# Optimization experiments

Hardware: AMD Instinct MI355X
Metric: run time of the kernel (lower is better)

## Reference

```python
import jax, jax.numpy as jnp
import numpy as np

B, T, C = 4, 2048, 1024
E = 8            # n_expert
K = 2            # n_expert_per_token
H = 1408         # moe_intermediate_size
HS = 1408 * 2    # shared expert intermediate (moe_intermediate_size * n_shared_expert)


def setup_inputs() -> dict:
    key = jax.random.key(0)
    k = jax.random.split(key, 8)
    s = 0.02
    return {
        "x":   jax.random.normal(k[0], (B, T, C), jnp.float32),
        "Wg":  jax.random.normal(k[1], (C, E), jnp.float32) * s,      # router gate
        "W1":  jax.random.normal(k[2], (E, C, H), jnp.float32) * s,   # fc_1 per expert
        "W2":  jax.random.normal(k[3], (E, C, H), jnp.float32) * s,   # fc_2 per expert
        "W3":  jax.random.normal(k[4], (E, H, C), jnp.float32) * s,   # proj per expert
        "Ws1": jax.random.normal(k[5], (C, HS), jnp.float32) * s,     # shared fc_1
        "Ws2": jax.random.normal(k[6], (C, HS), jnp.float32) * s,     # shared fc_2
        "Ws3": jax.random.normal(k[7], (HS, C), jnp.float32) * s,     # shared proj
    }


def reference(x, Wg, W1, W2, W3, Ws1, Ws2, Ws3):
    b, t, c = x.shape
    xf = x.reshape(-1, c)                       # [N, C]
    n = xf.shape[0]

    # Router: top-k then softmax over the selected logits (float32 softmax).
    router = xf @ Wg                            # [N, E]
    top_logits, idx = jax.lax.top_k(router, K)  # [N, K]
    probs = jax.nn.softmax(top_logits.astype(jnp.float32), axis=-1).astype(x.dtype)

    # token_expert_weights: scatter probs into dense [N, E] per-expert weights.
    w = jnp.zeros((n, E), x.dtype).at[jnp.arange(n)[:, None], idx].add(probs)

    # Per-expert gated MLP on all tokens; zero-weight tokens contribute nothing,
    # matching the masked gather/scatter-add of the original.
    h = jax.nn.silu(jnp.einsum('tc,ech->eth', xf, W1)) * jnp.einsum('tc,ech->eth', xf, W2)
    y = jnp.einsum('eth,ehc,te->tc', h, W3, w)  # weighted combine
    y = y.reshape(b, t, c)

    # Shared expert on the residual input.
    hs = jax.nn.silu(xf @ Ws1) * (xf @ Ws2)     # [N, HS]
    y = y + (hs @ Ws3).reshape(b, t, c)
    return y
```

## Files before the change

### kernel.cpp

```cpp
#include <hip/hip_runtime.h>
#include <cstdint>

#define NTOK 8192
#define CDIM 1024
#define HDIM 1408
#define HSDIM 2816
#define NEXP 8

typedef __attribute__((ext_vector_type(8))) short s8v;
typedef __attribute__((ext_vector_type(4))) float f4v;
typedef __attribute__((ext_vector_type(8))) unsigned short u16x8;

__device__ __forceinline__ unsigned short f2bf(float f) {
    unsigned int u = __float_as_uint(f);
    unsigned int r = (u + 0x7fffu + ((u >> 16) & 1u)) >> 16;
    return (unsigned short)r;
}
__device__ __forceinline__ float bf2f(unsigned short u) {
    return __uint_as_float(((unsigned int)u) << 16);
}

__device__ __forceinline__ void gld_lds16(const unsigned short* g, unsigned short* l) {
    __builtin_amdgcn_global_load_lds(
        (const __attribute__((address_space(1))) void*)g,
        (__attribute__((address_space(3))) void*)l, 16, 0, 0);
}


#define P_RTR 2048
#define P_CVT 8192
#define P_T1 (22 * 16 * 16)
#define P_T2 (16 * 22 * 8)
#define P_T3 (44 * 16 * 2)
#define P_T4 (16 * 44 * 1)
#define P_TOTAL (P_RTR + P_CVT + P_T1 + P_T2 + P_T3 + P_T4)

__device__ __forceinline__ void transpose_tile(
    float (*T)[68], const float* __restrict__ in, unsigned short* __restrict__ out,
    int R, int Cc, int bx, int by) {
    const int t = threadIdx.x;
    const int r0 = by * 64, c0 = bx * 64;
    {
        const int rl = t >> 2, cq = t & 3;
        const float* src = in + (size_t)(r0 + rl) * Cc + c0;
#pragma unroll
        for (int i = 0; i < 4; i++) {
            float4 v = *(const float4*)(src + (cq + 4 * i) * 4);
            *(float4*)&T[rl][(cq + 4 * i) * 4] = v;
        }
    }
    __syncthreads();
    {
        const int cl = t >> 2, rq = t & 3;
        unsigned short* dst = out + (size_t)(c0 + cl) * R + r0 + rq * 16;
        u16x8 lo, hi;
#pragma unroll
        for (int j = 0; j < 8; j++) lo[j] = f2bf(T[rq * 16 + j][cl]);
#pragma unroll
        for (int j = 0; j < 8; j++) hi[j] = f2bf(T[rq * 16 + 8 + j][cl]);
        *(u16x8*)dst = lo;
        *(u16x8*)(dst + 8) = hi;
    }
}

__global__ __launch_bounds__(256) void prep_kernel(
    const float* __restrict__ x, const float* __restrict__ Wg,
    const float* __restrict__ W1, const float* __restrict__ W2, const float* __restrict__ W3,
    const float* __restrict__ Ws1, const float* __restrict__ Ws2, const float* __restrict__ Ws3,
    unsigned short* __restrict__ xb,
    unsigned short* __restrict__ w1t, unsigned short* __restrict__ w2t,
    unsigned short* __restrict__ w3t,
    unsigned short* __restrict__ ws1t, unsigned short* __restrict__ ws2t,
    unsigned short* __restrict__ ws3t,
    int* __restrict__ idxK, float* __restrict__ probK, int* __restrict__ meta) {
    __shared__ float T[64][68];
    int bid = blockIdx.x;
    const int tid = threadIdx.x;

    if (bid < P_RTR) {
        const int t = bid * 4 + (tid >> 6);
        const int lane = tid & 63;
        const float* xr = x + (size_t)t * CDIM;
        float acc[NEXP];
#pragma unroll
        for (int e = 0; e < NEXP; e++) acc[e] = 0.f;
        for (int c = lane; c < CDIM; c += 64) {
            float xv = xr[c];
            const float* wr = Wg + c * NEXP;
#pragma unroll
            for (int e = 0; e < NEXP; e++) acc[e] += xv * wr[e];
        }
#pragma unroll
        for (int e = 0; e < NEXP; e++)
            for (int off = 32; off > 0; off >>= 1)
                acc[e] += __shfl_down(acc[e], off, 64);
        if (lane == 0) {
            int b0 = 0; float v0 = acc[0];
#pragma unroll
            for (int e = 1; e < NEXP; e++) if (acc[e] > v0) { v0 = acc[e]; b0 = e; }
            int b1 = -1; float v1 = -1e30f;
#pragma unroll
            for (int e = 0; e < NEXP; e++) if (e != b0 && acc[e] > v1) { v1 = acc[e]; b1 = e; }
            float p0 = 1.f / (1.f + __expf(v1 - v0));
            idxK[2 * t] = b0; idxK[2 * t + 1] = b1;
            probK[2 * t] = p0; probK[2 * t + 1] = 1.f - p0;
            atomicAdd(&meta[b0], 1);
            atomicAdd(&meta[b1], 1);
        }
        return;
    }
    bid -= P_RTR;
    if (bid < P_CVT) {
        const int i = bid * 256 + tid;
        float4 v = ((const float4*)x)[i];
        ushort4 o;
        o.x = f2bf(v.x); o.y = f2bf(v.y); o.z = f2bf(v.z); o.w = f2bf(v.w);
        ((ushort4*)xb)[i] = o;
        return;
    }
    bid -= P_CVT;
    if (bid < P_T1) {
        const int bx = bid % 22, by = (bid / 22) % 16, z = bid / (22 * 16);
        const float* in = (z < 8) ? W1 : W2;
        unsigned short* out = (z < 8) ? w1t : w2t;
        const int zz = (z < 8) ? z : z - 8;
        const size_t bs = (size_t)CDIM * HDIM;
        transpose_tile(T, in + zz * bs, out + zz * bs, CDIM, HDIM, bx, by);
        return;
    }
    bid -= P_T1;
    if (bid < P_T2) {
        const int bx = bid % 16, by = (bid / 16) % 22, z = bid / (16 * 22);
        const size_t bs = (size_t)HDIM * CDIM;
        transpose_tile(T, W3 + z * bs, w3t + z * bs, HDIM, CDIM, bx, by);
        return;
    }
    bid -= P_T2;
    if (bid < P_T3) {
        const int bx = bid % 44, by = (bid / 44) % 16, z = bid / (44 * 16);
        const float* in = (z == 0) ? Ws1 : Ws2;
        unsigned short* out = (z == 0) ? ws1t : ws2t;
        transpose_tile(T, in, out, CDIM, HSDIM, bx, by);
        return;
    }
    bid -= P_T3;
    {
        const int bx = bid % 16, by = bid / 16;
        transpose_tile(T, Ws3, ws3t, HSDIM, CDIM, bx, by);
    }
}

__global__ void offsets_kernel(int* meta) {
    int s = 0;
    for (int e = 0; e < NEXP; e++) { meta[8 + e] = s; meta[16 + e] = s; s += meta[e]; }
}

__global__ void fill_kernel(const int* __restrict__ idxK, const float* __restrict__ probK,
                            int* __restrict__ meta, int* __restrict__ rowT, float* __restrict__ rowW,
                            int* __restrict__ tokSlot) {
    int t = blockIdx.x * 256 + threadIdx.x;
    if (t >= NTOK) return;
#pragma unroll
    for (int k = 0; k < 2; k++) {
        int e = idxK[2 * t + k];
        int p = atomicAdd(&meta[16 + e], 1);
        rowT[p] = t;
        rowW[p] = probK[2 * t + k];
        tokSlot[2 * t + k] = p;
    }
}

__global__ __launch_bounds__(256) void gemm12_kernel(
    const unsigned short* __restrict__ xb,
    const unsigned short* __restrict__ w1, const unsigned short* __restrict__ w2,
    const unsigned short* __restrict__ ws1, const unsigned short* __restrict__ ws2,
    unsigned short* __restrict__ hE, unsigned short* __restrict__ hS,
    const int* __restrict__ rowT, const int* __restrict__ meta) {
    const int id = blockIdx.x;
    int z, m0, n0; bool SH;
    if (id < 3520) { SH = false; z = id & 7; int q = id >> 3; m0 = (q % 20) * 128; n0 = (q / 20) * 64; }
    else           { SH = true;  z = 8; int q = id - 3520; m0 = (q & 63) * 128; n0 = (q >> 6) * 64; }
    const int M = SH ? NTOK : meta[z];
    const int base = SH ? 0 : meta[8 + z];
    if (m0 >= M) return;

    const unsigned short* B1 = SH ? ws1 : w1 + (size_t)z * HDIM * CDIM;
    const unsigned short* B2 = SH ? ws2 : w2 + (size_t)z * HDIM * CDIM;

    __shared__ unsigned short L[16384];

    const int tid = threadIdx.x;
    const int srow = tid >> 2;
    const int key = (tid >> 3) & 3;
    const int co = ((tid & 3) ^ key) << 3;

    int am0 = m0 + srow;       am0 = am0 < M ? am0 : M - 1;
    int am1 = m0 + 64 + srow;  am1 = am1 < M ? am1 : M - 1;
    long ar0 = SH ? am0 : rowT[base + am0];
    long ar1 = SH ? am1 : rowT[base + am1];
    const unsigned short* a0p = xb + (size_t)ar0 * CDIM + co;
    const unsigned short* a1p = xb + (size_t)ar1 * CDIM + co;
    const unsigned short* b1p = B1 + (size_t)(n0 + srow) * CDIM + co;
    const unsigned short* b2p = B2 + (size_t)(n0 + srow) * CDIM + co;

    const int w = tid >> 6, lane = tid & 63;
    const int wm = (w >> 1) * 64, wn = (w & 1) * 32;
    const int quad = lane >> 4, l15 = lane & 15;
    const int rcx = (quad ^ ((l15 >> 1) & 3)) << 3;

    f4v acc1[4][2], acc2[4][2];
#pragma unroll
    for (int i = 0; i < 4; i++)
#pragma unroll
        for (int j = 0; j < 2; j++) {
            f4v zz = {0.f, 0.f, 0.f, 0.f};
            acc1[i][j] = zz; acc2[i][j] = zz;
        }

#define STAGE12(b, k0) do { \
        gld_lds16(a0p + (k0), L + (b) * 4096 + tid * 8); \
        gld_lds16(a1p + (k0), L + (b) * 4096 + 2048 + tid * 8); \
        gld_lds16(b1p + (k0), L + 8192 + (b) * 2048 + tid * 8); \
        gld_lds16(b2p + (k0), L + 12288 + (b) * 2048 + tid * 8); } while (0)

    auto compute = [&](int b) {
        const unsigned short* Ab = L + b * 4096;
        const unsigned short* B1b = L + 8192 + b * 2048;
        const unsigned short* B2b = L + 12288 + b * 2048;
        s8v af[4], bf1[2], bf2[2];
#pragma unroll
        for (int mt = 0; mt < 4; mt++)
            af[mt] = *(const s8v*)(Ab + (wm + mt * 16 + l15) * 32 + rcx);
#pragma unroll
        for (int nt = 0; nt < 2; nt++) {
            bf1[nt] = *(const s8v*)(B1b + (wn + nt * 16 + l15) * 32 + rcx);
            bf2[nt] = *(const s8v*)(B2b + (wn + nt * 16 + l15) * 32 + rcx);
        }
#pragma unroll
        for (int mt = 0; mt < 4; mt++)
#pragma unroll
            for (int nt = 0; nt < 2; nt++) {
                acc1[mt][nt] = __builtin_amdgcn_mfma_f32_16x16x32_bf16(af[mt], bf1[nt], acc1[mt][nt], 0, 0, 0);
                acc2[mt][nt] = __builtin_amdgcn_mfma_f32_16x16x32_bf16(af[mt], bf2[nt], acc2[mt][nt], 0, 0, 0);
            }
    };

    const int NS = CDIM / 32;
    STAGE12(0, 0);
    __syncthreads();
#pragma unroll 1
    for (int ks = 0; ks < NS; ks++) {
        if (ks + 1 < NS) STAGE12((ks + 1) & 1, (ks + 1) * 32);
        compute(ks & 1);
        __syncthreads();
    }
#undef STAGE12

#pragma unroll
    for (int mt = 0; mt < 4; mt++) {
#pragma unroll
        for (int r = 0; r < 4; r++) {
            int gm = m0 + wm + mt * 16 + quad * 4 + r;
            if (gm < M) {
                unsigned short* hrow = SH ? hS + (size_t)gm * HSDIM
                                          : hE + (size_t)(base + gm) * HDIM;
#pragma unroll
                for (int nt = 0; nt < 2; nt++) {
                    float z1 = acc1[mt][nt][r];
                    float z2 = acc2[mt][nt][r];
                    float hv = (z1 / (1.f + __expf(-z1))) * z2;
                    hrow[n0 + wn + nt * 16 + l15] = f2bf(hv);
                }
            }
        }
    }
}

__global__ __launch_bounds__(256) void gemm3_kernel(
    const unsigned short* __restrict__ hE, const unsigned short* __restrict__ hS,
    const unsigned short* __restrict__ w3, const unsigned short* __restrict__ ws3,
    float* __restrict__ Out, unsigned short* __restrict__ pE,
    const int* __restrict__ rowT, const float* __restrict__ rowW, const int* __restrict__ meta) {
    const int id = blockIdx.x;
    int z, m0, n0; bool SH;
    if (id < 512) { SH = true;  z = 8; int q = id; m0 = (q & 63) * 128; n0 = (q >> 6) * 128; }
    else          { SH = false; int r = id - 512; z = r & 7; int q = r >> 3; m0 = (q % 20) * 128; n0 = (q / 20) * 128; }
    const int M = SH ? NTOK : meta[z];
    const int base = SH ? 0 : meta[8 + z];
    if (m0 >= M) return;
    const int K = SH ? HSDIM : HDIM;
    const unsigned short* A = SH ? hS : hE;
    const unsigned short* B = SH ? ws3 : w3 + (size_t)z * CDIM * HDIM;

    __shared__ unsigned short L[16384];

    const int tid = threadIdx.x;
    const int srow = tid >> 2;
    const int key = (tid >> 3) & 3;
    const int co = ((tid & 3) ^ key) << 3;

    int am0 = m0 + srow;       am0 = am0 < M ? am0 : M - 1;
    int am1 = m0 + 64 + srow;  am1 = am1 < M ? am1 : M - 1;
    const unsigned short* a0p = A + (size_t)(base + am0) * K + co;
    const unsigned short* a1p = A + (size_t)(base + am1) * K + co;
    const unsigned short* b0p = B + (size_t)(n0 + srow) * K + co;
    const unsigned short* b1p = B + (size_t)(n0 + 64 + srow) * K + co;

    const int w = tid >> 6, lane = tid & 63;
    const int wm = (w >> 1) * 64, wn = (w & 1) * 64;
    const int quad = lane >> 4, l15 = lane & 15;
    const int rcx = (quad ^ ((l15 >> 1) & 3)) << 3;

    f4v acc[4][4];
#pragma unroll
    for (int i = 0; i < 4; i++)
#pragma unroll
        for (int j = 0; j < 4; j++) {
            f4v zz = {0.f, 0.f, 0.f, 0.f};
            acc[i][j] = zz;
        }

#define STAGE3(b, k0) do { \
        gld_lds16(a0p + (k0), L + (b) * 4096 + tid * 8); \
        gld_lds16(a1p + (k0), L + (b) * 4096 + 2048 + tid * 8); \
        gld_lds16(b0p + (k0), L + 8192 + (b) * 4096 + tid * 8); \
        gld_lds16(b1p + (k0), L + 8192 + (b) * 4096 + 2048 + tid * 8); } while (0)

    auto compute = [&](int b) {
        const unsigned short* Ab = L + b * 4096;
        const unsigned short* Bb = L + 8192 + b * 4096;
        s8v af[4], bf[4];
#pragma unroll
        for (int mt = 0; mt < 4; mt++)
            af[mt] = *(const s8v*)(Ab + (wm + mt * 16 + l15) * 32 + rcx);
#pragma unroll
        for (int nt = 0; nt < 4; nt++)
            bf[nt] = *(const s8v*)(Bb + (wn + nt * 16 + l15) * 32 + rcx);
#pragma unroll
        for (int mt = 0; mt < 4; mt++)
#pragma unroll
            for (int nt = 0; nt < 4; nt++)
                acc[mt][nt] = __builtin_amdgcn_mfma_f32_16x16x32_bf16(af[mt], bf[nt], acc[mt][nt], 0, 0, 0);
    };

    const int NS = K / 32;
    STAGE3(0, 0);
    __syncthreads();
#pragma unroll 1
    for (int ks = 0; ks < NS; ks++) {
        if (ks + 1 < NS) STAGE3((ks + 1) & 1, (ks + 1) * 32);
        compute(ks & 1);
        __syncthreads();
    }
#undef STAGE3

#pragma unroll
    for (int mt = 0; mt < 4; mt++) {
#pragma unroll
        for (int r = 0; r < 4; r++) {
            int gm = m0 + wm + mt * 16 + quad * 4 + r;
            if (gm < M) {
                if (SH) {
                    size_t o = (size_t)gm * CDIM + n0 + wn + l15;
#pragma unroll
                    for (int nt = 0; nt < 4; nt++)
                        Out[o + nt * 16] = acc[mt][nt][r];
                } else {
                    size_t o = (size_t)(base + gm) * CDIM + n0 + wn + l15;
#pragma unroll
                    for (int nt = 0; nt < 4; nt++)
                        pE[o + nt * 16] = f2bf(acc[mt][nt][r]);
                }
            }
        }
    }
}

__global__ __launch_bounds__(256) void combine_kernel(
    float* __restrict__ Out, const unsigned short* __restrict__ pE,
    const int* __restrict__ tokSlot, const float* __restrict__ rowW) {
    const int t = blockIdx.x;
    const int c = threadIdx.x * 4;
    const int s0 = tokSlot[2 * t], s1 = tokSlot[2 * t + 1];
    const float w0 = rowW[s0], w1 = rowW[s1];
    float* op = Out + (size_t)t * CDIM + c;
    float4 o = *(float4*)op;
    ushort4 a = *(const ushort4*)(pE + (size_t)s0 * CDIM + c);
    ushort4 b = *(const ushort4*)(pE + (size_t)s1 * CDIM + c);
    o.x += w0 * bf2f(a.x) + w1 * bf2f(b.x);
    o.y += w0 * bf2f(a.y) + w1 * bf2f(b.y);
    o.z += w0 * bf2f(a.z) + w1 * bf2f(b.z);
    o.w += w0 * bf2f(a.w) + w1 * bf2f(b.w);
    *(float4*)op = o;
}


extern "C" void kernel_launch(void* const* d_in, const int* in_sizes, int n_in,
                              void* d_out, int out_size, void* d_ws, size_t ws_size,
                              hipStream_t stream) {
    const float* x   = (const float*)d_in[0];
    const float* Wg  = (const float*)d_in[1];
    const float* W1  = (const float*)d_in[2];
    const float* W2  = (const float*)d_in[3];
    const float* W3  = (const float*)d_in[4];
    const float* Ws1 = (const float*)d_in[5];
    const float* Ws2 = (const float*)d_in[6];
    const float* Ws3 = (const float*)d_in[7];
    float* out = (float*)d_out;

    char* p = (char*)d_ws;
    auto carve = [&](size_t bytes) {
        char* r = p;
        p += (bytes + 255) & ~(size_t)255;
        return r;
    };
    unsigned short* xb   = (unsigned short*)carve((size_t)NTOK * CDIM * 2);
    unsigned short* w1t  = (unsigned short*)carve((size_t)NEXP * HDIM * CDIM * 2);
    unsigned short* w2t  = (unsigned short*)carve((size_t)NEXP * HDIM * CDIM * 2);
    unsigned short* w3t  = (unsigned short*)carve((size_t)NEXP * CDIM * HDIM * 2);
    unsigned short* ws1t = (unsigned short*)carve((size_t)HSDIM * CDIM * 2);
    unsigned short* ws2t = (unsigned short*)carve((size_t)HSDIM * CDIM * 2);
    unsigned short* ws3t = (unsigned short*)carve((size_t)CDIM * HSDIM * 2);
    unsigned short* hE   = (unsigned short*)carve((size_t)2 * NTOK * HDIM * 2);
    unsigned short* hS   = (unsigned short*)carve((size_t)NTOK * HSDIM * 2);
    int*   idxK   = (int*)carve((size_t)NTOK * 2 * 4);
    float* probK  = (float*)carve((size_t)NTOK * 2 * 4);
    int*   rowT   = (int*)carve((size_t)2 * NTOK * 4);
    float* rowW   = (float*)carve((size_t)2 * NTOK * 4);
    int*   tokSlot= (int*)carve((size_t)2 * NTOK * 4);
    int*   meta   = (int*)carve(256);

    unsigned short* pE = w1t;

    hipMemsetAsync(meta, 0, 256, stream);
    prep_kernel<<<P_TOTAL, 256, 0, stream>>>(
        x, Wg, W1, W2, W3, Ws1, Ws2, Ws3,
        xb, w1t, w2t, w3t, ws1t, ws2t, ws3t, idxK, probK, meta);
    offsets_kernel<<<1, 1, 0, stream>>>(meta);
    fill_kernel<<<NTOK / 256, 256, 0, stream>>>(idxK, probK, meta, rowT, rowW, tokSlot);

    gemm12_kernel<<<3520 + 2816, 256, 0, stream>>>(
        xb, w1t, w2t, ws1t, ws2t, hE, hS, rowT, meta);
    gemm3_kernel<<<512 + 1280, 256, 0, stream>>>(
        hE, hS, w3t, ws3t, out, pE, rowT, rowW, meta);
    combine_kernel<<<NTOK, 256, 0, stream>>>(out, pE, tokSlot, rowW);
}
```

Before: 826.4 us.

## Rewrite gate/up GEMM with 256x128 tiles, 512 threads and ping-pong pipelining

The fused fc1/fc2 GEMM moves from 128x64 tiles with 256 threads to 256x128 tiles with 512 threads. W1 and W2 rows are interleaved in 16-column groups so one accumulator array covers both projections. K steps widen to 64, and a double-buffered 64KB LDS schedule interleaves sub-tile loads with MFMA phases using explicit barriers, waitcnts and s_setprio. The aim is more data reuse per loaded byte and better overlap of global loads with matrix math. The cost is higher register and LDS pressure, fewer blocks for load balance on small experts, and fragile hand-written synchronisation.

```diff
diff --git a/kernel.cpp b/kernel.cpp
--- a/kernel.cpp
+++ b/kernel.cpp
@@ -170,7 +170,7 @@
     }
 }
 
-__global__ __launch_bounds__(256) void gemm12_kernel(
+__global__ __launch_bounds__(512, 2) void gemm12_kernel(
     const unsigned short* __restrict__ xb,
     const unsigned short* __restrict__ w1, const unsigned short* __restrict__ w2,
     const unsigned short* __restrict__ ws1, const unsigned short* __restrict__ ws2,
@@ -178,8 +178,8 @@
     const int* __restrict__ rowT, const int* __restrict__ meta) {
     const int id = blockIdx.x;
     int z, m0, n0; bool SH;
-    if (id < 3520) { SH = false; z = id & 7; int q = id >> 3; m0 = (q % 20) * 128; n0 = (q / 20) * 64; }
-    else           { SH = true;  z = 8; int q = id - 3520; m0 = (q & 63) * 128; n0 = (q >> 6) * 64; }
+    if (id < 880) { SH = false; z = id & 7; int q = id >> 3; m0 = (q % 10) * 256; n0 = (q / 10) * 128; }
+    else          { SH = true;  z = 8; int q = id - 880; m0 = (q & 31) * 256; n0 = (q >> 5) * 128; }
     const int M = SH ? NTOK : meta[z];
     const int base = SH ? 0 : meta[8 + z];
     if (m0 >= M) return;
@@ -187,89 +187,136 @@
     const unsigned short* B1 = SH ? ws1 : w1 + (size_t)z * HDIM * CDIM;
     const unsigned short* B2 = SH ? ws2 : w2 + (size_t)z * HDIM * CDIM;
 
-    __shared__ unsigned short L[16384];
+    __shared__ unsigned short L[65536];
 
     const int tid = threadIdx.x;
-    const int srow = tid >> 2;
-    const int key = (tid >> 3) & 3;
-    const int co = ((tid & 3) ^ key) << 3;
-
-    int am0 = m0 + srow;       am0 = am0 < M ? am0 : M - 1;
-    int am1 = m0 + 64 + srow;  am1 = am1 < M ? am1 : M - 1;
-    long ar0 = SH ? am0 : rowT[base + am0];
-    long ar1 = SH ? am1 : rowT[base + am1];
-    const unsigned short* a0p = xb + (size_t)ar0 * CDIM + co;
-    const unsigned short* a1p = xb + (size_t)ar1 * CDIM + co;
-    const unsigned short* b1p = B1 + (size_t)(n0 + srow) * CDIM + co;
-    const unsigned short* b2p = B2 + (size_t)(n0 + srow) * CDIM + co;
+    const int srow = tid >> 3;
+    const int cg = ((tid & 7) ^ (srow & 7)) << 3;
+
+    const unsigned short* pA[2][2];
+    const unsigned short* pB[2][2];
+#pragma unroll
+    for (int h = 0; h < 2; h++)
+#pragma unroll
+        for (int u = 0; u < 2; u++) {
+            int lr = h * 128 + u * 64 + srow;
+            int am = m0 + lr; am = am < M ? am : M - 1;
+            int gr = SH ? am : rowT[base + am];
+            pA[h][u] = xb + (size_t)gr * CDIM + cg;
+            int n = lr;
+            int hcol = n0 + ((n >> 5) << 4) + (n & 15);
+            pB[h][u] = (((n >> 4) & 1) ? B2 : B1) + (size_t)hcol * CDIM + cg;
+        }
 
     const int w = tid >> 6, lane = tid & 63;
-    const int wm = (w >> 1) * 64, wn = (w & 1) * 32;
+    const int wr = w >> 2, wc = w & 3;
     const int quad = lane >> 4, l15 = lane & 15;
-    const int rcx = (quad ^ ((l15 >> 1) & 3)) << 3;
-
-    f4v acc1[4][2], acc2[4][2];
-#pragma unroll
-    for (int i = 0; i < 4; i++)
-#pragma unroll
-        for (int j = 0; j < 2; j++) {
+    int ck[2];
+    ck[0] = (quad ^ (l15 & 7)) << 3;
+    ck[1] = ((4 + quad) ^ (l15 & 7)) << 3;
+    const int ArdBase = wr * 8192 + l15 * 64;
+    const int BrdBase = 16384 + (wc >> 1) * 8192 + ((wc & 1) * 64 + l15) * 64;
+
+    f4v acc[8][4];
+#pragma unroll
+    for (int i = 0; i < 8; i++)
+#pragma unroll
+        for (int j = 0; j < 4; j++) {
             f4v zz = {0.f, 0.f, 0.f, 0.f};
-            acc1[i][j] = zz; acc2[i][j] = zz;
-        }
-
-#define STAGE12(b, k0) do { \
-        gld_lds16(a0p + (k0), L + (b) * 4096 + tid * 8); \
-        gld_lds16(a1p + (k0), L + (b) * 4096 + 2048 + tid * 8); \
-        gld_lds16(b1p + (k0), L + 8192 + (b) * 2048 + tid * 8); \
-        gld_lds16(b2p + (k0), L + 12288 + (b) * 2048 + tid * 8); } while (0)
-
-    auto compute = [&](int b) {
-        const unsigned short* Ab = L + b * 4096;
-        const unsigned short* B1b = L + 8192 + b * 2048;
-        const unsigned short* B2b = L + 12288 + b * 2048;
-        s8v af[4], bf1[2], bf2[2];
-#pragma unroll
-        for (int mt = 0; mt < 4; mt++)
-            af[mt] = *(const s8v*)(Ab + (wm + mt * 16 + l15) * 32 + rcx);
-#pragma unroll
-        for (int nt = 0; nt < 2; nt++) {
-            bf1[nt] = *(const s8v*)(B1b + (wn + nt * 16 + l15) * 32 + rcx);
-            bf2[nt] = *(const s8v*)(B2b + (wn + nt * 16 + l15) * 32 + rcx);
-        }
-#pragma unroll
-        for (int mt = 0; mt < 4; mt++)
-#pragma unroll
-            for (int nt = 0; nt < 2; nt++) {
-                acc1[mt][nt] = __builtin_amdgcn_mfma_f32_16x16x32_bf16(af[mt], bf1[nt], acc1[mt][nt], 0, 0, 0);
-                acc2[mt][nt] = __builtin_amdgcn_mfma_f32_16x16x32_bf16(af[mt], bf2[nt], acc2[mt][nt], 0, 0, 0);
-            }
-    };
-
-    const int NS = CDIM / 32;
-    STAGE12(0, 0);
-    __syncthreads();
+            acc[i][j] = zz;
+        }
+
+    s8v aF[4][2], bF[2][2];
+
+    auto SA = [&](int s, int h, int kt) {
+        gld_lds16(pA[h][0] + (size_t)kt * 64, L + s * 32768 + h * 8192 + tid * 8);
+        gld_lds16(pA[h][1] + (size_t)kt * 64, L + s * 32768 + h * 8192 + 4096 + tid * 8);
+    };
+    auto SB = [&](int s, int h, int kt) {
+        gld_lds16(pB[h][0] + (size_t)kt * 64, L + s * 32768 + 16384 + h * 8192 + tid * 8);
+        gld_lds16(pB[h][1] + (size_t)kt * 64, L + s * 32768 + 16384 + h * 8192 + 4096 + tid * 8);
+    };
+    auto RA = [&](int s, int mb) {
+#pragma unroll
+        for (int j = 0; j < 4; j++)
+#pragma unroll
+            for (int k = 0; k < 2; k++)
+                aF[j][k] = *(const s8v*)(L + s * 32768 + ArdBase + (mb + j) * 1024 + ck[k]);
+    };
+    auto RB = [&](int s, int nb) {
+#pragma unroll
+        for (int j = 0; j < 2; j++)
+#pragma unroll
+            for (int k = 0; k < 2; k++)
+                bF[j][k] = *(const s8v*)(L + s * 32768 + BrdBase + (nb + j) * 1024 + ck[k]);
+    };
+    auto MF = [&](int mb, int nb) {
+#pragma unroll
+        for (int k = 0; k < 2; k++)
+#pragma unroll
+            for (int j = 0; j < 4; j++)
+#pragma unroll
+                for (int n = 0; n < 2; n++)
+                    acc[mb + j][nb + n] = __builtin_amdgcn_mfma_f32_16x16x32_bf16(
+                        aF[j][k], bF[n][k], acc[mb + j][nb + n], 0, 0, 0);
+    };
+
+#define BAR() __builtin_amdgcn_s_barrier()
+#define LGKM0() do { asm volatile("s_waitcnt lgkmcnt(0)" ::: "memory"); \
+                     __builtin_amdgcn_sched_barrier(0); } while (0)
+#define VM2() do { asm volatile("s_waitcnt vmcnt(2)" ::: "memory"); \
+                   __builtin_amdgcn_sched_barrier(0); } while (0)
+#define PRIO1() __builtin_amdgcn_s_setprio(1)
+#define PRIO0() __builtin_amdgcn_s_setprio(0)
+
+    SA(0, 0, 0); SA(0, 1, 0); SB(0, 0, 0); SB(0, 1, 0); SA(1, 0, 1);
+    VM2(); BAR();
+
 #pragma unroll 1
-    for (int ks = 0; ks < NS; ks++) {
-        if (ks + 1 < NS) STAGE12((ks + 1) & 1, (ks + 1) * 32);
-        compute(ks & 1);
-        __syncthreads();
-    }
-#undef STAGE12
-
-#pragma unroll
-    for (int mt = 0; mt < 4; mt++) {
+    for (int i = 0; i < 8; i++) {
+        const int k1 = 2 * i + 1;
+        const int k2 = (2 * i + 2 < 16) ? 2 * i + 2 : 15;
+        const int k3 = (2 * i + 3 < 16) ? 2 * i + 3 : 15;
+        RA(0, 0); RB(0, 0); SA(1, 1, k1);
+        BAR(); LGKM0(); PRIO1(); MF(0, 0); PRIO0(); BAR();
+        RB(0, 2); SB(1, 0, k1);
+        BAR(); LGKM0(); PRIO1(); MF(0, 2); PRIO0(); BAR();
+        RA(0, 4); RB(0, 0); SB(1, 1, k1);
+        BAR(); LGKM0(); PRIO1(); MF(4, 0); PRIO0(); BAR();
+        RB(0, 2); SA(0, 0, k2);
+        BAR(); LGKM0(); PRIO1(); MF(4, 2); PRIO0(); VM2(); BAR();
+        RA(1, 0); RB(1, 0); SA(0, 1, k2);
+        BAR(); LGKM0(); PRIO1(); MF(0, 0); PRIO0(); BAR();
+        RB(1, 2); SB(0, 0, k2);
+        BAR(); LGKM0(); PRIO1(); MF(0, 2); PRIO0(); BAR();
+        RA(1, 4); RB(1, 0); SB(0, 1, k2);
+        BAR(); LGKM0(); PRIO1(); MF(4, 0); PRIO0(); BAR();
+        RB(1, 2); SA(1, 0, k3);
+        BAR(); LGKM0(); PRIO1(); MF(4, 2); PRIO0(); VM2(); BAR();
+    }
+    asm volatile("s_waitcnt vmcnt(0)" ::: "memory");
+
+#undef BAR
+#undef LGKM0
+#undef VM2
+#undef PRIO1
+#undef PRIO0
+
+#pragma unroll
+    for (int mf = 0; mf < 8; mf++) {
 #pragma unroll
         for (int r = 0; r < 4; r++) {
-            int gm = m0 + wm + mt * 16 + quad * 4 + r;
+            int gm = m0 + wr * 128 + mf * 16 + quad * 4 + r;
             if (gm < M) {
                 unsigned short* hrow = SH ? hS + (size_t)gm * HSDIM
                                           : hE + (size_t)(base + gm) * HDIM;
-#pragma unroll
-                for (int nt = 0; nt < 2; nt++) {
-                    float z1 = acc1[mt][nt][r];
-                    float z2 = acc2[mt][nt][r];
+                const int cbase = n0 + wc * 32;
+#pragma unroll
+                for (int p = 0; p < 2; p++) {
+                    float z1 = acc[mf][2 * p][r];
+                    float z2 = acc[mf][2 * p + 1][r];
                     float hv = (z1 / (1.f + __expf(-z1))) * z2;
-                    hrow[n0 + wn + nt * 16 + l15] = f2bf(hv);
+                    hrow[cbase + p * 16 + l15] = f2bf(hv);
                 }
             }
         }
@@ -439,7 +486,7 @@
     offsets_kernel<<<1, 1, 0, stream>>>(meta);
     fill_kernel<<<NTOK / 256, 256, 0, stream>>>(idxK, probK, meta, rowT, rowW, tokSlot);
 
-    gemm12_kernel<<<3520 + 2816, 256, 0, stream>>>(
+    gemm12_kernel<<<880 + 704, 512, 0, stream>>>(
         xb, w1t, w2t, ws1t, ws2t, hE, hS, rowT, meta);
     gemm3_kernel<<<512 + 1280, 256, 0, stream>>>(
         hE, hS, w3t, ws3t, out, pE, rowT, rowW, meta);
```

New measurement: 810.2 us. -2.0%, faster.
